# Kernel optimization log

Hardware: AMD Instinct MI355X
Metric: run time of the kernel (lower is better)

Reference implementation:

```python
import jax, jax.numpy as jnp
import numpy as np

N, DX, DS, NLAB, NSMAT = 20000, 16, 64, 10, 64
E_HALF = 160000
E = 2 * E_HALF
N_LABELED = 2000
N_HIDDEN = 6  # six Linear(nsmat,nsmat) layers between input and output layers


def setup_inputs() -> dict:
    key = jax.random.key(0)
    ks = jax.random.split(key, 16)
    xembed = jax.random.normal(ks[0], (N, DX), jnp.float32)
    sembed = jax.random.normal(ks[1], (N, DS), jnp.float32)
    # ylprob are log-probabilities (original uses exp(ylprob) in the KL term)
    ylprob = jax.nn.log_softmax(jax.random.normal(ks[2], (N, NLAB), jnp.float32), axis=1)
    # build edge list with explicit reverse pairs so loss_orth is exercised
    s_half = jax.random.randint(ks[3], (E_HALF,), 0, N, jnp.int32)
    t_half = jax.random.randint(ks[4], (E_HALF,), 0, N, jnp.int32)
    src = jnp.concatenate([s_half, t_half])
    tgt = jnp.concatenate([t_half, s_half])
    edge_w = jax.random.uniform(ks[5], (E,), jnp.float32, 0.1, 1.0)
    rev1 = jnp.arange(E_HALF, dtype=jnp.int32)
    rev2 = rev1 + E_HALF
    idvert = jax.random.randint(ks[6], (N_LABELED,), 0, N, jnp.int32)
    fcW_in = jax.random.normal(ks[7], (2 * DS, NSMAT), jnp.float32) / np.sqrt(2 * DS)
    fcb_in = jnp.zeros((NSMAT,), jnp.float32)
    fcW_h = jax.random.normal(ks[8], (N_HIDDEN, NSMAT, NSMAT), jnp.float32) / np.sqrt(NSMAT)
    fcb_h = jnp.zeros((N_HIDDEN, NSMAT), jnp.float32)
    fcW_out = jax.random.normal(ks[9], (NSMAT, DX * DX), jnp.float32) / np.sqrt(NSMAT)
    fcb_out = jnp.zeros((DX * DX,), jnp.float32)
    # cl_smat params: Linear(dimx, nlab) + LogSoftmax
    clW = jax.random.normal(ks[10], (DX, NLAB), jnp.float32) / np.sqrt(DX)
    clb = jnp.zeros((NLAB,), jnp.float32)
    return dict(xembed=xembed, sembed=sembed, ylprob=ylprob, edge_w=edge_w,
                fcW_in=fcW_in, fcb_in=fcb_in, fcW_h=fcW_h, fcb_h=fcb_h,
                fcW_out=fcW_out, fcb_out=fcb_out, clW=clW, clb=clb,
                src=src, tgt=tgt, rev1=rev1, rev2=rev2, idvert=idvert)


def _edge_matrices(sf, tf, fcW_in, fcb_in, fcW_h, fcb_h, fcW_out, fcb_out):
    # [E, 2*dims] -> 8-layer ReLU MLP -> [E, dimx, dimx]
    h = jax.nn.relu(jnp.concatenate([sf, tf], axis=1) @ fcW_in + fcb_in)
    for i in range(N_HIDDEN):
        h = jax.nn.relu(h @ fcW_h[i] + fcb_h[i])
    return (h @ fcW_out + fcb_out).reshape(-1, DX, DX)


def reference(xembed, sembed, ylprob, edge_w, fcW_in, fcb_in, fcW_h, fcb_h,
              fcW_out, fcb_out, clW, clb, src, tgt, rev1, rev2, idvert):
    # per-edge sheaf transport matrices from gathered structure embeddings
    edge_mats = _edge_matrices(sembed[src], sembed[tgt],
                               fcW_in, fcb_in, fcW_h, fcb_h, fcW_out, fcb_out)

    # orthogonality loss over reverse edge pairs: mean RMS(A@B - I) * dimx
    prod = jnp.einsum('eij,ejk->eik', edge_mats[rev1], edge_mats[rev2])
    diff = prod - jnp.eye(DX, dtype=prod.dtype)
    loss_orth = jnp.mean(jnp.sqrt(jnp.mean(diff * diff, axis=(1, 2)) * (DX * DX)))

    # message passing: gather -> bmm -> weighted scatter-add -> degree normalize
    messages = jnp.einsum('eij,ej->ei', edge_mats, xembed[src])  # [E, dimx]
    weighted = messages * edge_w[:, None]
    new_x = jax.ops.segment_sum(weighted, tgt, num_segments=N)   # [N, dimx]
    deg = jax.ops.segment_sum(edge_w, tgt, num_segments=N)       # [N]
    xmaped = jnp.where((deg > 0)[:, None], new_x / jnp.maximum(deg, 1e-20)[:, None], new_x)

    loss_smap = jnp.mean((xmaped - xembed) ** 2) * DX

    # KL(y || g) on labeled nodes; cl_smat = Linear + LogSoftmax
    glprob = jax.nn.log_softmax(xmaped[idvert] @ clW + clb, axis=1)
    ylp = ylprob[idvert]
    loss_lbpr = jnp.mean(jnp.sum(jnp.exp(ylp) * (ylp - glprob), axis=1))

    # original recomputes the same MLP on the same inputs and takes the MSE of
    # two identical tensors -> exactly zero (and zero gradient)
    loss_cons = jnp.zeros((), xembed.dtype)

    return (loss_orth, loss_cons, loss_smap, loss_lbpr)
```

## Files before the change

### kernel.cpp

```cpp
#include <hip/hip_runtime.h>
#include <hip/hip_bf16.h>

#define N_NODES   20000
#define DX        16
#define DS        64
#define NLAB      10
#define NSMAT     64
#define E_HALF    160000
#define E_TOT     320000
#define N_LABELED 2000
#define N_HIDDEN  6

#define PAIRS 32
#define NT    (E_HALF / PAIRS)

typedef short bf16x8 __attribute__((ext_vector_type(8)));
typedef float f32x4  __attribute__((ext_vector_type(4)));
#define MFMA16(a, b, c) __builtin_amdgcn_mfma_f32_16x16x32_bf16((a), (b), (c), 0, 0, 0)

#define LDS_A0    0
#define LDS_H0    16384
#define LDS_H1    24576
#define LDS_MT    24576
#define LDS_TOTAL 40960

#define WS_W0     0
#define WS_WH     16384
#define WS_WOUT   65536
#define WS_FLOATS 98304

__device__ __forceinline__ unsigned short f2bf(float f) {
    unsigned int u = __float_as_uint(f);
    unsigned int r = (u + 0x7fffu + ((u >> 16) & 1u)) >> 16;
    return (unsigned short)r;
}
__device__ __forceinline__ unsigned int cvtpk(float lo, float hi) {
    unsigned int r;
    asm("v_cvt_pk_bf16_f32 %0, %1, %2" : "=v"(r) : "v"(lo), "v"(hi));
    return r;
}
__device__ __forceinline__ float bflo(unsigned int u) { return __uint_as_float(u << 16); }
__device__ __forceinline__ float bfhi(unsigned int u) { return __uint_as_float(u & 0xffff0000u); }

__global__ void k_prep(const float* __restrict__ Win, const float* __restrict__ Wh,
                       const float* __restrict__ Wout, unsigned short* __restrict__ wsw) {
    const int idx = blockIdx.x * 256 + threadIdx.x;
    if (idx >= 49152) return;
    float val; int base, KK, k, n;
    if (idx < 8192) {
        k = idx >> 6; n = idx & 63; val = Win[idx]; base = WS_W0 / 2; KK = 4;
    } else if (idx < 32768) {
        const int r = idx - 8192; const int l = r >> 12; const int rr = r & 4095;
        k = rr >> 6; n = rr & 63; val = Wh[r]; base = (WS_WH + l * 8192) / 2; KK = 2;
    } else {
        const int r = idx - 32768; k = r >> 8; n = r & 255;
        val = Wout[r]; base = WS_WOUT / 2; KK = 2;
    }
    const int ntile = n >> 4, kk = k >> 5, hi = (k >> 3) & 3, j = k & 7;
    const int lane = hi * 16 + (n & 15);
    wsw[base + (((ntile * KK + kk) * 64 + lane) * 8 + j)] = f2bf(val);
}

__global__ void k_zero(float* __restrict__ p, int n) {
    int i = blockIdx.x * blockDim.x + threadIdx.x;
    const int stride = gridDim.x * blockDim.x;
    for (; i < n; i += stride) p[i] = 0.0f;
}

__global__ __launch_bounds__(256, 4) void k_main(
    const float* __restrict__ xembed, const float* __restrict__ sembed,
    const float* __restrict__ edge_w,
    const float* __restrict__ bin, const float* __restrict__ bh,
    const float* __restrict__ bout,
    const int* __restrict__ src, const int* __restrict__ tgt,
    const unsigned short* __restrict__ wsw,
    float* __restrict__ newx, float* __restrict__ deg,
    float* __restrict__ orth_part)
{
    extern __shared__ char lds[];
    const int tid    = threadIdx.x;
    const int lane   = tid & 63;
    const int wv     = tid >> 6;
    const int lane15 = lane & 15;
    const int hi     = lane >> 4;
    const int p0     = blockIdx.x * PAIRS;

    float4 sx;
    {
        const int si = tid >> 3, sc = tid & 7;
        const bool sT = (sc >= 4); const int scc = sc & 3;
        const int p = p0 + si;
        const int nodeA = sT ? tgt[p] : src[p];
        const float4* nrow = (const float4*)(sembed + (size_t)nodeA * DS + scc * 16);
        const float4 v0 = nrow[0], v1 = nrow[1], v2 = nrow[2], v3 = nrow[3];
        const int colA = (sT ? 128 : 0) + scc * 32;
        const int colB = (sT ? 0 : 128) + scc * 32;
        const int sXor = (si & 7) << 4;
        uint2 pk;
        pk.x = cvtpk(v0.x, v0.y); pk.y = cvtpk(v0.z, v0.w);
        *(uint2*)(lds + LDS_A0 + si * 256 + ((colA + 0) ^ sXor)) = pk;
        *(uint2*)(lds + LDS_A0 + (32 + si) * 256 + ((colB + 0) ^ sXor)) = pk;
        pk.x = cvtpk(v1.x, v1.y); pk.y = cvtpk(v1.z, v1.w);
        *(uint2*)(lds + LDS_A0 + si * 256 + ((colA + 8) ^ sXor)) = pk;
        *(uint2*)(lds + LDS_A0 + (32 + si) * 256 + ((colB + 8) ^ sXor)) = pk;
        pk.x = cvtpk(v2.x, v2.y); pk.y = cvtpk(v2.z, v2.w);
        *(uint2*)(lds + LDS_A0 + si * 256 + ((colA + 16) ^ sXor)) = pk;
        *(uint2*)(lds + LDS_A0 + (32 + si) * 256 + ((colB + 16) ^ sXor)) = pk;
        pk.x = cvtpk(v3.x, v3.y); pk.y = cvtpk(v3.z, v3.w);
        *(uint2*)(lds + LDS_A0 + si * 256 + ((colA + 24) ^ sXor)) = pk;
        *(uint2*)(lds + LDS_A0 + (32 + si) * 256 + ((colB + 24) ^ sXor)) = pk;

        const int sed = tid >> 2, sqq = tid & 3;
        const int nodeX = (sed < 32) ? src[p0 + sed] : tgt[p0 + sed - 32];
        sx = *(const float4*)(xembed + (size_t)nodeX * DX + sqq * 4);
    }

    float bin_r[4];
    #pragma unroll
    for (int n = 0; n < 4; ++n) bin_r[n] = bin[16 * n + lane15];

    const int arow = 16 * wv + lane15;
    const int axor = (arow & 7) << 4;

    __syncthreads();

    {
        bf16x8 a[4];
        #pragma unroll
        for (int kk = 0; kk < 4; ++kk)
            a[kk] = *(const bf16x8*)(lds + LDS_A0 + arow * 256 + ((kk * 64 + hi * 16) ^ axor));
        const unsigned short* w0g = wsw + WS_W0 / 2;
        #pragma unroll
        for (int n = 0; n < 4; ++n) {
            f32x4 acc = {0.0f, 0.0f, 0.0f, 0.0f};
            #pragma unroll
            for (int kk = 0; kk < 4; ++kk) {
                const bf16x8 b = *(const bf16x8*)(w0g + ((n * 4 + kk) * 64 + lane) * 8);
                acc = MFMA16(a[kk], b, acc);
            }
            #pragma unroll
            for (int r = 0; r < 4; ++r) {
                const int row = 16 * wv + 4 * hi + r;
                *(__hip_bfloat16*)(lds + LDS_H0 + row * 128 +
                    (((16 * n + lane15) * 2) ^ ((row & 7) << 4))) =
                    __float2bfloat16(fmaxf(acc[r] + bin_r[n], 0.0f));
            }
        }
    }
    __syncthreads();

    float bcur[4], bnxt[4];
    {
        const float* bl = bh + lane15;
        bcur[0] = bl[0]; bcur[1] = bl[16]; bcur[2] = bl[32]; bcur[3] = bl[48];
    }
    #pragma unroll
    for (int l = 0; l < N_HIDDEN; ++l) {
        if (l + 1 < N_HIDDEN) {
            const float* bl = bh + (l + 1) * 64 + lane15;
            bnxt[0] = bl[0]; bnxt[1] = bl[16]; bnxt[2] = bl[32]; bnxt[3] = bl[48];
        }
        const int sB = (l & 1) ? LDS_H1 : LDS_H0;
        const int dB = (l & 1) ? LDS_H0 : LDS_H1;
        const unsigned short* whg = wsw + WS_WH / 2 + l * 4096;
        const bf16x8 a0 = *(const bf16x8*)(lds + sB + arow * 128 + ((hi * 16) ^ axor));
        const bf16x8 a1 = *(const bf16x8*)(lds + sB + arow * 128 + ((64 + hi * 16) ^ axor));
        #pragma unroll
        for (int n = 0; n < 4; ++n) {
            f32x4 acc = {0.0f, 0.0f, 0.0f, 0.0f};
            const bf16x8 b0 = *(const bf16x8*)(whg + ((n * 2 + 0) * 64 + lane) * 8);
            const bf16x8 b1 = *(const bf16x8*)(whg + ((n * 2 + 1) * 64 + lane) * 8);
            acc = MFMA16(a0, b0, acc);
            acc = MFMA16(a1, b1, acc);
            #pragma unroll
            for (int r = 0; r < 4; ++r) {
                const int row = 16 * wv + 4 * hi + r;
                *(__hip_bfloat16*)(lds + dB + row * 128 +
                    (((16 * n + lane15) * 2) ^ ((row & 7) << 4))) =
                    __float2bfloat16(fmaxf(acc[r] + bcur[n], 0.0f));
            }
        }
        bcur[0] = bnxt[0]; bcur[1] = bnxt[1]; bcur[2] = bnxt[2]; bcur[3] = bnxt[3];
    }
    __syncthreads();

    {
        float bo[16];
        #pragma unroll
        for (int n = 0; n < 16; ++n) bo[n] = bout[16 * n + lane15];

        const bf16x8 a0 = *(const bf16x8*)(lds + LDS_H0 + arow * 128 + ((hi * 16) ^ axor));
        const bf16x8 a1 = *(const bf16x8*)(lds + LDS_H0 + arow * 128 + ((64 + hi * 16) ^ axor));
        const unsigned short* wog = wsw + WS_WOUT / 2;
        #pragma unroll
        for (int n = 0; n < 16; ++n) {
            const bf16x8 b0 = *(const bf16x8*)(wog + ((n * 2 + 0) * 64 + lane) * 8);
            const bf16x8 b1 = *(const bf16x8*)(wog + ((n * 2 + 1) * 64 + lane) * 8);
            f32x4 acc = {0.0f, 0.0f, 0.0f, 0.0f};
            acc = MFMA16(a0, b0, acc);
            acc = MFMA16(a1, b1, acc);
            #pragma unroll
            for (int r = 0; r < 4; ++r) {
                const int row = 16 * wv + 4 * hi + r;
                const __hip_bfloat16 mv = __float2bfloat16(acc[r] + bo[n]);
                if (wv < 2) {
                    const int i = row;
                    *(__hip_bfloat16*)(lds + LDS_A0 + i * 512 +
                        (((n * 16 + lane15) * 2) ^ ((i & 7) << 4))) = mv;
                } else {
                    const int i = row - 32;
                    *(__hip_bfloat16*)(lds + LDS_MT + i * 512 +
                        (((lane15 * 16 + n) * 2) ^ ((i & 7) << 4))) = mv;
                }
            }
        }
    }
    __syncthreads();

    {
        const int e = tid >> 2, q = tid & 3;
        const int i = e & 31;
        const bool isB = (e >= 32);
        float xv[16];
        #pragma unroll
        for (int qq = 0; qq < 4; ++qq) {
            xv[4 * qq + 0] = __shfl(sx.x, qq, 4);
            xv[4 * qq + 1] = __shfl(sx.y, qq, 4);
            xv[4 * qq + 2] = __shfl(sx.z, qq, 4);
            xv[4 * qq + 3] = __shfl(sx.w, qq, 4);
        }
        const int p = p0 + i;
        const float w_e  = isB ? edge_w[p + E_HALF] : edge_w[p];
        const int target = isB ? src[p] : tgt[p];
        const int ixor = (i & 7) << 4;
        if (!isB) {
            #pragma unroll
            for (int jj = 0; jj < 4; ++jj) {
                const int row = 4 * q + jj;
                const uint4 m0 = *(const uint4*)(lds + LDS_A0 + i * 512 + ((row * 32) ^ ixor));
                const uint4 m1 = *(const uint4*)(lds + LDS_A0 + i * 512 + ((row * 32 + 16) ^ ixor));
                float m = bflo(m0.x) * xv[0];
                m = fmaf(bfhi(m0.x), xv[1], m);  m = fmaf(bflo(m0.y), xv[2], m);
                m = fmaf(bfhi(m0.y), xv[3], m);  m = fmaf(bflo(m0.z), xv[4], m);
                m = fmaf(bfhi(m0.z), xv[5], m);  m = fmaf(bflo(m0.w), xv[6], m);
                m = fmaf(bfhi(m0.w), xv[7], m);  m = fmaf(bflo(m1.x), xv[8], m);
                m = fmaf(bfhi(m1.x), xv[9], m);  m = fmaf(bflo(m1.y), xv[10], m);
                m = fmaf(bfhi(m1.y), xv[11], m); m = fmaf(bflo(m1.z), xv[12], m);
                m = fmaf(bfhi(m1.z), xv[13], m); m = fmaf(bflo(m1.w), xv[14], m);
                m = fmaf(bfhi(m1.w), xv[15], m);
                atomicAdd(&newx[(size_t)target * DX + row], w_e * m);
            }
        } else {
            float macc[4] = {0.f, 0.f, 0.f, 0.f};
            #pragma unroll
            for (int c = 0; c < 16; ++c) {
                const uint2 v = *(const uint2*)(lds + LDS_MT + i * 512 + ((c * 32 + q * 8) ^ ixor));
                const float xc = xv[c];
                macc[0] = fmaf(bflo(v.x), xc, macc[0]);
                macc[1] = fmaf(bfhi(v.x), xc, macc[1]);
                macc[2] = fmaf(bflo(v.y), xc, macc[2]);
                macc[3] = fmaf(bfhi(v.y), xc, macc[3]);
            }
            #pragma unroll
            for (int jj = 0; jj < 4; ++jj)
                atomicAdd(&newx[(size_t)target * DX + 4 * q + jj], w_e * macc[jj]);
        }
        if (q == 0) atomicAdd(&deg[target], w_e);
    }

    float wsum = 0.0f;
    {
        const bf16x8 zf = {0, 0, 0, 0, 0, 0, 0, 0};
        #pragma unroll
        for (int pp = 0; pp < 8; ++pp) {
            const int pi = 8 * wv + pp;
            const int pxor = (pi & 7) << 4;
            const int off = (lane15 * 32 + (hi & 1) * 16) ^ pxor;
            bf16x8 af  = *(const bf16x8*)(lds + LDS_A0 + pi * 512 + off);
            bf16x8 bfr = *(const bf16x8*)(lds + LDS_MT + pi * 512 + off);
            if (hi >= 2) { af = zf; bfr = zf; }
            f32x4 pr = {0.f, 0.f, 0.f, 0.f};
            pr = MFMA16(af, bfr, pr);
            float ss = 0.0f;
            #pragma unroll
            for (int r = 0; r < 4; ++r) {
                const float d = pr[r] - ((4 * hi + r == lane15) ? 1.0f : 0.0f);
                ss = fmaf(d, d, ss);
            }
            #pragma unroll
            for (int o = 32; o > 0; o >>= 1) ss += __shfl_xor(ss, o, 64);
            wsum += sqrtf(ss);
        }
    }
    __syncthreads();
    if (lane == 0) ((float*)(lds + LDS_A0))[wv] = wsum;
    __syncthreads();
    if (tid == 0) {
        const float* pw = (const float*)(lds + LDS_A0);
        atomicAdd(&orth_part[blockIdx.x & 255], pw[0] + pw[1] + pw[2] + pw[3]);
    }
}

__device__ __forceinline__ float block_reduce_256(float v) {
    __shared__ float part[4];
    #pragma unroll
    for (int off = 32; off > 0; off >>= 1) v += __shfl_xor(v, off, 64);
    const int lane = threadIdx.x & 63, wid = threadIdx.x >> 6;
    if (lane == 0) part[wid] = v;
    __syncthreads();
    float s = 0.0f;
    if (threadIdx.x == 0) {
        #pragma unroll
        for (int i = 0; i < 4; ++i) s += part[i];
    }
    return s;
}

__global__ __launch_bounds__(256) void k_smap(
    const float* __restrict__ xembed, float* __restrict__ nx,
    const float* __restrict__ deg, float* __restrict__ accum)
{
    const int n = blockIdx.x * 256 + threadIdx.x;
    float ss = 0.0f;
    if (n < N_NODES) {
        const float d = deg[n];
        const float inv = 1.0f / fmaxf(d, 1e-20f);
        #pragma unroll
        for (int c = 0; c < DX; ++c) {
            const float v  = nx[(size_t)n * DX + c];
            const float xm = (d > 0.0f) ? v * inv : v;
            nx[(size_t)n * DX + c] = xm;
            const float df = xm - xembed[(size_t)n * DX + c];
            ss = fmaf(df, df, ss);
        }
    }
    ss = block_reduce_256(ss);
    if (threadIdx.x == 0) atomicAdd(&accum[1], ss);
}

__global__ __launch_bounds__(256) void k_lbpr(
    const float* __restrict__ ylprob, const float* __restrict__ xmaped,
    const float* __restrict__ clW, const float* __restrict__ clb,
    const int* __restrict__ idvert, float* __restrict__ accum)
{
    const int v = blockIdx.x * 256 + threadIdx.x;
    float kl = 0.0f;
    if (v < N_LABELED) {
        const int n = idvert[v];
        float z[NLAB];
        #pragma unroll
        for (int c = 0; c < NLAB; ++c) z[c] = clb[c];
        #pragma unroll
        for (int i = 0; i < DX; ++i) {
            const float xi = xmaped[(size_t)n * DX + i];
            #pragma unroll
            for (int c = 0; c < NLAB; ++c) z[c] = fmaf(xi, clW[i * NLAB + c], z[c]);
        }
        float mx = z[0];
        #pragma unroll
        for (int c = 1; c < NLAB; ++c) mx = fmaxf(mx, z[c]);
        float se = 0.0f;
        #pragma unroll
        for (int c = 0; c < NLAB; ++c) se += expf(z[c] - mx);
        const float lse = mx + logf(se);
        #pragma unroll
        for (int c = 0; c < NLAB; ++c) {
            const float yl = ylprob[(size_t)n * NLAB + c];
            kl += expf(yl) * (yl - (z[c] - lse));
        }
    }
    kl = block_reduce_256(kl);
    if (threadIdx.x == 0) atomicAdd(&accum[2], kl);
}

__global__ __launch_bounds__(256) void k_final(
    const float* __restrict__ accum, const float* __restrict__ orth_part,
    float* __restrict__ out)
{
    float v = orth_part[threadIdx.x];
    v = block_reduce_256(v);
    if (threadIdx.x == 0) {
        out[0] = v * (1.0f / (float)E_HALF);
        out[1] = 0.0f;
        out[2] = accum[1] * (1.0f / (float)N_NODES);
        out[3] = accum[2] * (1.0f / (float)N_LABELED);
    }
}

extern "C" void kernel_launch(void* const* d_in, const int* in_sizes, int n_in,
                              void* d_out, int out_size, void* d_ws, size_t ws_size,
                              hipStream_t stream) {
    const float* xembed = (const float*)d_in[0];
    const float* sembed = (const float*)d_in[1];
    const float* ylprob = (const float*)d_in[2];
    const float* edge_w = (const float*)d_in[3];
    const float* Win    = (const float*)d_in[4];
    const float* bin    = (const float*)d_in[5];
    const float* Wh     = (const float*)d_in[6];
    const float* bh     = (const float*)d_in[7];
    const float* Wout   = (const float*)d_in[8];
    const float* bout   = (const float*)d_in[9];
    const float* clW    = (const float*)d_in[10];
    const float* clb    = (const float*)d_in[11];
    const int*   src    = (const int*)d_in[12];
    const int*   tgt    = (const int*)d_in[13];
    const int*   idvert = (const int*)d_in[16];

    unsigned short* wsw = (unsigned short*)d_ws;
    float* wsF       = (float*)((char*)d_ws + WS_FLOATS);
    float* newx      = wsF;
    float* deg       = wsF + (size_t)N_NODES * DX;
    float* accum     = deg + N_NODES;
    float* orth_part = accum + 4;
    const int nzero = N_NODES * DX + N_NODES + 4 + 256;

    k_prep<<<192, 256, 0, stream>>>(Win, Wh, Wout, wsw);
    k_zero<<<512, 256, 0, stream>>>(wsF, nzero);

    k_main<<<NT, 256, LDS_TOTAL, stream>>>(
        xembed, sembed, edge_w, bin, bh, bout, src, tgt, wsw, newx, deg, orth_part);

    k_smap<<<(N_NODES + 255) / 256, 256, 0, stream>>>(xembed, newx, deg, accum);
    k_lbpr<<<(N_LABELED + 255) / 256, 256, 0, stream>>>(ylprob, newx, clW, clb, idvert, accum);
    k_final<<<1, 256, 0, stream>>>(accum, orth_part, (float*)d_out);
}
```

Measured before the change: 143.4 us.

## Shrink LDS footprint, widen swizzle, and pack transposed edge-matrix stores

The transposed edge-matrix buffer now overlaps the hidden-activation region, so total LDS per block drops from 40 KB to 32 KB and the launch bound moves to 5 blocks per SIMD group. The final-layer A fragments are read into registers before the barrier so that region can be overwritten safely. The swizzle also folds in row bit 3 plus a column-dependent XOR to cut bank conflicts. Waves writing the transposed matrices now pack results into bf16 pairs and issue 16-byte stores instead of scattered 2-byte stores. The trade-off is more register pressure under the tighter launch bound and more complex address arithmetic, and any mismatch between the swizzles used for writes and reads would corrupt results.

```diff
diff --git a/kernel.cpp b/kernel.cpp
--- a/kernel.cpp
+++ b/kernel.cpp
@@ -21,8 +21,11 @@
 #define LDS_A0    0
 #define LDS_H0    16384
 #define LDS_H1    24576
-#define LDS_MT    24576
-#define LDS_TOTAL 40960
+#define LDS_MT    16384
+#define LDS_TOTAL 32768
+
+#define SWZ(row)  ((((row) & 7) << 4) ^ (((row) & 8) << 2))
+#define CSP(c)    (((c) & 12) << 2)
 
 #define WS_W0     0
 #define WS_WH     16384
@@ -67,7 +70,7 @@
     for (; i < n; i += stride) p[i] = 0.0f;
 }
 
-__global__ __launch_bounds__(256, 4) void k_main(
+__global__ __launch_bounds__(256, 5) void k_main(
     const float* __restrict__ xembed, const float* __restrict__ sembed,
     const float* __restrict__ edge_w,
     const float* __restrict__ bin, const float* __restrict__ bh,
@@ -95,7 +98,7 @@
         const float4 v0 = nrow[0], v1 = nrow[1], v2 = nrow[2], v3 = nrow[3];
         const int colA = (sT ? 128 : 0) + scc * 32;
         const int colB = (sT ? 0 : 128) + scc * 32;
-        const int sXor = (si & 7) << 4;
+        const int sXor = SWZ(si);
         uint2 pk;
         pk.x = cvtpk(v0.x, v0.y); pk.y = cvtpk(v0.z, v0.w);
         *(uint2*)(lds + LDS_A0 + si * 256 + ((colA + 0) ^ sXor)) = pk;
@@ -120,7 +123,7 @@
     for (int n = 0; n < 4; ++n) bin_r[n] = bin[16 * n + lane15];
 
     const int arow = 16 * wv + lane15;
-    const int axor = (arow & 7) << 4;
+    const int axor = SWZ(arow);
 
     __syncthreads();
 
@@ -142,7 +145,7 @@
             for (int r = 0; r < 4; ++r) {
                 const int row = 16 * wv + 4 * hi + r;
                 *(__hip_bfloat16*)(lds + LDS_H0 + row * 128 +
-                    (((16 * n + lane15) * 2) ^ ((row & 7) << 4))) =
+                    (((16 * n + lane15) * 2) ^ SWZ(row))) =
                     __float2bfloat16(fmaxf(acc[r] + bin_r[n], 0.0f));
             }
         }
@@ -176,12 +179,15 @@
             for (int r = 0; r < 4; ++r) {
                 const int row = 16 * wv + 4 * hi + r;
                 *(__hip_bfloat16*)(lds + dB + row * 128 +
-                    (((16 * n + lane15) * 2) ^ ((row & 7) << 4))) =
+                    (((16 * n + lane15) * 2) ^ SWZ(row))) =
                     __float2bfloat16(fmaxf(acc[r] + bcur[n], 0.0f));
             }
         }
         bcur[0] = bnxt[0]; bcur[1] = bnxt[1]; bcur[2] = bnxt[2]; bcur[3] = bnxt[3];
     }
+
+    const bf16x8 fa0 = *(const bf16x8*)(lds + LDS_H0 + arow * 128 + ((hi * 16) ^ axor));
+    const bf16x8 fa1 = *(const bf16x8*)(lds + LDS_H0 + arow * 128 + ((64 + hi * 16) ^ axor));
     __syncthreads();
 
     {
@@ -189,29 +195,53 @@
         #pragma unroll
         for (int n = 0; n < 16; ++n) bo[n] = bout[16 * n + lane15];
 
-        const bf16x8 a0 = *(const bf16x8*)(lds + LDS_H0 + arow * 128 + ((hi * 16) ^ axor));
-        const bf16x8 a1 = *(const bf16x8*)(lds + LDS_H0 + arow * 128 + ((64 + hi * 16) ^ axor));
         const unsigned short* wog = wsw + WS_WOUT / 2;
-        #pragma unroll
-        for (int n = 0; n < 16; ++n) {
-            const bf16x8 b0 = *(const bf16x8*)(wog + ((n * 2 + 0) * 64 + lane) * 8);
-            const bf16x8 b1 = *(const bf16x8*)(wog + ((n * 2 + 1) * 64 + lane) * 8);
-            f32x4 acc = {0.0f, 0.0f, 0.0f, 0.0f};
-            acc = MFMA16(a0, b0, acc);
-            acc = MFMA16(a1, b1, acc);
+        if (wv < 2) {
+            #pragma unroll
+            for (int n = 0; n < 16; ++n) {
+                const bf16x8 b0 = *(const bf16x8*)(wog + ((n * 2 + 0) * 64 + lane) * 8);
+                const bf16x8 b1 = *(const bf16x8*)(wog + ((n * 2 + 1) * 64 + lane) * 8);
+                f32x4 acc = {0.0f, 0.0f, 0.0f, 0.0f};
+                acc = MFMA16(fa0, b0, acc);
+                acc = MFMA16(fa1, b1, acc);
+                #pragma unroll
+                for (int r = 0; r < 4; ++r) {
+                    const int i = 16 * wv + 4 * hi + r;
+                    *(__hip_bfloat16*)(lds + LDS_A0 + i * 512 +
+                        (((n * 16 + lane15) * 2) ^ SWZ(i))) =
+                        __float2bfloat16(acc[r] + bo[n]);
+                }
+            }
+        } else {
+            unsigned int pk0[8], pk1[8], pk2[8], pk3[8];
+            float tmp0 = 0.f, tmp1 = 0.f, tmp2 = 0.f, tmp3 = 0.f;
+            #pragma unroll
+            for (int n = 0; n < 16; ++n) {
+                const bf16x8 b0 = *(const bf16x8*)(wog + ((n * 2 + 0) * 64 + lane) * 8);
+                const bf16x8 b1 = *(const bf16x8*)(wog + ((n * 2 + 1) * 64 + lane) * 8);
+                f32x4 acc = {0.0f, 0.0f, 0.0f, 0.0f};
+                acc = MFMA16(fa0, b0, acc);
+                acc = MFMA16(fa1, b1, acc);
+                const float v0 = acc[0] + bo[n], v1 = acc[1] + bo[n];
+                const float v2 = acc[2] + bo[n], v3 = acc[3] + bo[n];
+                if (n & 1) {
+                    pk0[n >> 1] = cvtpk(tmp0, v0); pk1[n >> 1] = cvtpk(tmp1, v1);
+                    pk2[n >> 1] = cvtpk(tmp2, v2); pk3[n >> 1] = cvtpk(tmp3, v3);
+                } else {
+                    tmp0 = v0; tmp1 = v1; tmp2 = v2; tmp3 = v3;
+                }
+            }
+            const int csp = CSP(lane15);
             #pragma unroll
             for (int r = 0; r < 4; ++r) {
-                const int row = 16 * wv + 4 * hi + r;
-                const __hip_bfloat16 mv = __float2bfloat16(acc[r] + bo[n]);
-                if (wv < 2) {
-                    const int i = row;
-                    *(__hip_bfloat16*)(lds + LDS_A0 + i * 512 +
-                        (((n * 16 + lane15) * 2) ^ ((i & 7) << 4))) = mv;
-                } else {
-                    const int i = row - 32;
-                    *(__hip_bfloat16*)(lds + LDS_MT + i * 512 +
-                        (((lane15 * 16 + n) * 2) ^ ((i & 7) << 4))) = mv;
-                }
+                const int i = 16 * (wv - 2) + 4 * hi + r;
+                const int sw = SWZ(i) ^ csp;
+                char* base = lds + LDS_MT + i * 512;
+                const unsigned int* pkr = (r == 0) ? pk0 : (r == 1) ? pk1 : (r == 2) ? pk2 : pk3;
+                *(uint4*)(base + ((lane15 * 32 + 0) ^ sw)) =
+                    make_uint4(pkr[0], pkr[1], pkr[2], pkr[3]);
+                *(uint4*)(base + ((lane15 * 32 + 16) ^ sw)) =
+                    make_uint4(pkr[4], pkr[5], pkr[6], pkr[7]);
             }
         }
     }
@@ -232,7 +262,7 @@
         const int p = p0 + i;
         const float w_e  = isB ? edge_w[p + E_HALF] : edge_w[p];
         const int target = isB ? src[p] : tgt[p];
-        const int ixor = (i & 7) << 4;
+        const int ixor = SWZ(i);
         if (!isB) {
             #pragma unroll
             for (int jj = 0; jj < 4; ++jj) {
@@ -254,7 +284,8 @@
             float macc[4] = {0.f, 0.f, 0.f, 0.f};
             #pragma unroll
             for (int c = 0; c < 16; ++c) {
-                const uint2 v = *(const uint2*)(lds + LDS_MT + i * 512 + ((c * 32 + q * 8) ^ ixor));
+                const uint2 v = *(const uint2*)(lds + LDS_MT + i * 512 +
+                                                ((c * 32 + q * 8) ^ ixor ^ CSP(c)));
                 const float xc = xv[c];
                 macc[0] = fmaf(bflo(v.x), xc, macc[0]);
                 macc[1] = fmaf(bfhi(v.x), xc, macc[1]);
@@ -274,10 +305,11 @@
         #pragma unroll
         for (int pp = 0; pp < 8; ++pp) {
             const int pi = 8 * wv + pp;
-            const int pxor = (pi & 7) << 4;
-            const int off = (lane15 * 32 + (hi & 1) * 16) ^ pxor;
-            bf16x8 af  = *(const bf16x8*)(lds + LDS_A0 + pi * 512 + off);
-            bf16x8 bfr = *(const bf16x8*)(lds + LDS_MT + pi * 512 + off);
+            const int pxor = SWZ(pi);
+            const int offA = (lane15 * 32 + (hi & 1) * 16) ^ pxor;
+            const int offB = (lane15 * 32 + (hi & 1) * 16) ^ pxor ^ CSP(lane15);
+            bf16x8 af  = *(const bf16x8*)(lds + LDS_A0 + pi * 512 + offA);
+            bf16x8 bfr = *(const bf16x8*)(lds + LDS_MT + pi * 512 + offB);
             if (hi >= 2) { af = zf; bfr = zf; }
             f32x4 pr = {0.f, 0.f, 0.f, 0.f};
             pr = MFMA16(af, bfr, pr);
```

After: 156.7 us. 1.09x slower.
